# Kernel tuning notes

Measured on AMD Instinct MI355X. Metric: run time of the kernel, lower is better.

The kernel has to match this reference:

```python
import jax, jax.numpy as jnp
import numpy as np

N = 8192
IN_F = 512
OUT_F = 256

def setup_inputs() -> dict:
    key = jax.random.key(0)
    k1, k2, k3 = jax.random.split(key, 3)
    A = jax.random.uniform(k1, (N, N), dtype=jnp.float32)
    X = jax.random.normal(k2, (N, IN_F), dtype=jnp.float32)
    init_range = np.sqrt(6.0 / (IN_F + OUT_F)).astype(np.float32)
    W = jax.random.uniform(k3, (IN_F, OUT_F), dtype=jnp.float32,
                           minval=-init_range, maxval=init_range)
    return {"weighted_adjacency_matrix": A, "feature_matrix": X, "weight": W}

def reference(weighted_adjacency_matrix, feature_matrix, weight):
    A = weighted_adjacency_matrix
    # d = (1 + row_sum(A))^{-1/2}; D^{-1/2} A D^{-1/2} via row/col broadcast scaling
    d = jax.lax.rsqrt(1.0 + jnp.sum(A, axis=1))            # [N]
    norm_adj = d[:, None] * A * d[None, :]                  # [N, N]
    support = feature_matrix @ weight                       # [N, out_features]
    return norm_adj @ support                               # [N, out_features]
```

## Files before the change

kernel.cpp:

```cpp
#include <hip/hip_runtime.h>
#include <hip/hip_bf16.h>
#include <stdint.h>

#define NROW 8192
#define INF  512
#define OUTF 256

typedef __attribute__((ext_vector_type(8))) short bf16x8;
typedef __attribute__((ext_vector_type(4))) float f32x4;

__device__ __forceinline__ unsigned short f2bf(float x) {
  union { float f; unsigned u; } v; v.f = x;
  unsigned r = v.u + 0x7fffu + ((v.u >> 16) & 1u);
  return (unsigned short)(r >> 16);
}
__device__ __forceinline__ unsigned short f2bf_fast(float x) {
  union { float f; unsigned u; } v; v.f = x;
  return (unsigned short)((v.u + 0x8000u) >> 16);
}
__device__ __forceinline__ float bf2f(unsigned short h) {
  union { unsigned u; float f; } v; v.u = ((unsigned)h) << 16;
  return v.f;
}

__device__ __forceinline__ void async_cp16(const void* g, void* l) {
  __builtin_amdgcn_global_load_lds((const __attribute__((address_space(1))) void*)g,
                                   (__attribute__((address_space(3))) void*)l,
                                   16, 0, 0);
}

__global__ __launch_bounds__(256) void k_rowsum(
    const float* __restrict__ A, float* __restrict__ dv) {
  int w = threadIdx.x >> 6, lane = threadIdx.x & 63;
  int row = blockIdx.x * 4 + w;
  const float4* ar = (const float4*)(A + (size_t)row * NROW);
  float s = 0.f;
  #pragma unroll 4
  for (int it = 0; it < NROW / 256; ++it) {
    float4 v = ar[it * 64 + lane];
    s += (v.x + v.y) + (v.z + v.w);
  }
  #pragma unroll
  for (int off = 32; off > 0; off >>= 1) s += __shfl_down(s, off, 64);
  if (lane == 0) dv[row] = rsqrtf(1.f + s);
}

__global__ __launch_bounds__(256) void k_convert_w(
    const float* __restrict__ W, unsigned short* __restrict__ WsT) {
  int idx = blockIdx.x * 256 + threadIdx.x;
  int k = idx >> 8, f = idx & 255;
  WsT[(size_t)f * INF + k] = f2bf(W[idx]);
}

__global__ __launch_bounds__(256, 2) void k_support_fx(
    const unsigned short* __restrict__ WsT,
    const float* __restrict__ X,
    const float* __restrict__ dv,
    unsigned short* __restrict__ YT) {
  __shared__ unsigned short lA[128 * 64];
  __shared__ unsigned short lB[128 * 64];
  const int t = threadIdx.x;
  const int w = t >> 6, lane = t & 63;
  const int m0 = blockIdx.x * 128;
  const int n0 = blockIdx.y * 128;
  const int rsub = lane >> 3, csub = lane & 7, swz = csub ^ rsub;
  const int lr = lane & 15, lq = lane >> 4, x7 = lane & 7;
  const int mw = (w >> 1) * 64, nw = (w & 1) * 64;

  const int xrow = t >> 1, xhalf = t & 1;
  const float4* xsrc = (const float4*)(X + (size_t)(n0 + xrow) * INF + xhalf * 32);

  f32x4 acc[4][4];
  #pragma unroll
  for (int i = 0; i < 4; ++i)
    #pragma unroll
    for (int j = 0; j < 4; ++j) acc[i][j] = f32x4{0.f, 0.f, 0.f, 0.f};

  const unsigned short* ga0 = WsT + (size_t)(m0 + w * 8 + rsub) * INF + swz * 8;

  for (int it = 0; it < INF / 64; ++it) {
    __syncthreads();
    #pragma unroll
    for (int i = 0; i < 4; ++i)
      async_cp16(ga0 + (size_t)(i * 32) * INF + it * 64, &lA[(i * 32 + w * 8) * 64]);
    #pragma unroll
    for (int u = 0; u < 8; ++u) {
      float4 v = xsrc[it * 16 + u];
      ushort4 b;
      b.x = f2bf(v.x); b.y = f2bf(v.y); b.z = f2bf(v.z); b.w = f2bf(v.w);
      int k = xhalf * 32 + u * 4;
      int chunk = k >> 3, klo = k & 7;
      int slot = chunk ^ (xrow & 7);
      *(ushort4*)&lB[xrow * 64 + (slot << 3) + klo] = b;
    }
    __syncthreads();
    #pragma unroll
    for (int ks = 0; ks < 2; ++ks) {
      bf16x8 af[4], bfv[4];
      #pragma unroll
      for (int mi = 0; mi < 4; ++mi)
        af[mi] = *(const bf16x8*)&lA[(mw + mi * 16 + lr) * 64 + (((ks * 4 + lq) ^ x7) << 3)];
      #pragma unroll
      for (int ni = 0; ni < 4; ++ni)
        bfv[ni] = *(const bf16x8*)&lB[(nw + ni * 16 + lr) * 64 + (((ks * 4 + lq) ^ x7) << 3)];
      #pragma unroll
      for (int mi = 0; mi < 4; ++mi)
        #pragma unroll
        for (int ni = 0; ni < 4; ++ni)
          acc[mi][ni] = __builtin_amdgcn_mfma_f32_16x16x32_bf16(
              af[mi], bfv[ni], acc[mi][ni], 0, 0, 0);
    }
  }
  #pragma unroll
  for (int mi = 0; mi < 4; ++mi) {
    #pragma unroll
    for (int ni = 0; ni < 4; ++ni) {
      f32x4 a = acc[mi][ni];
      int gr0 = m0 + mw + mi * 16 + lq * 4;
      int gc  = n0 + nw + ni * 16 + lr;
      float dd = dv[gc];
      #pragma unroll
      for (int r = 0; r < 4; ++r)
        YT[(size_t)(gr0 + r) * NROW + gc] = f2bf(dd * a[r]);
    }
  }
}

__global__ __launch_bounds__(256, 2) void k_gemm_main_f32a(
    const float* __restrict__ A,
    const unsigned short* __restrict__ YT,
    unsigned short* __restrict__ P) {
  __shared__ unsigned short lA[128 * 64];
  __shared__ unsigned short lB[256 * 64];
  const int t = threadIdx.x;
  const int w = t >> 6, lane = t & 63;
  const int m0 = blockIdx.x * 128;
  const int kz = blockIdx.y * 1024;
  const int rsub = lane >> 3, csub = lane & 7, swz = csub ^ rsub;
  const int lr = lane & 15, lq = lane >> 4, x7 = lane & 7;
  const int mw = (w & 1) * 64;
  const int nw = (w >> 1) * 128;

  const int arow = t >> 2, aq = t & 3;
  const int aklo = (aq & 1) * 4;

  f32x4 acc[4][8];
  #pragma unroll
  for (int i = 0; i < 4; ++i)
    #pragma unroll
    for (int j = 0; j < 8; ++j) acc[i][j] = f32x4{0.f, 0.f, 0.f, 0.f};

  const unsigned short* gb0 = YT + (size_t)(w * 8 + rsub) * NROW + kz + swz * 8;

  for (int it = 0; it < 16; ++it) {
    __syncthreads();
    #pragma unroll
    for (int i = 0; i < 8; ++i)
      async_cp16(gb0 + (size_t)(i * 32) * NROW + it * 64, &lB[(i * 32 + w * 8) * 64]);
    #pragma unroll
    for (int h = 0; h < 2; ++h) {
      int r = arow + h * 64;
      const float4* asrc = (const float4*)(A + (size_t)(m0 + r) * NROW + kz + it * 64);
      #pragma unroll
      for (int j = 0; j < 4; ++j) {
        float4 v = asrc[aq + 4 * j];
        ushort4 b;
        b.x = f2bf_fast(v.x); b.y = f2bf_fast(v.y);
        b.z = f2bf_fast(v.z); b.w = f2bf_fast(v.w);
        int chunk = (aq + 4 * j) >> 1;
        int slot = chunk ^ (r & 7);
        *(ushort4*)&lA[r * 64 + (slot << 3) + aklo] = b;
      }
    }
    __syncthreads();
    #pragma unroll
    for (int ks = 0; ks < 2; ++ks) {
      bf16x8 af[4], bfv[8];
      #pragma unroll
      for (int mi = 0; mi < 4; ++mi)
        af[mi] = *(const bf16x8*)&lA[(mw + mi * 16 + lr) * 64 + (((ks * 4 + lq) ^ x7) << 3)];
      #pragma unroll
      for (int ni = 0; ni < 8; ++ni)
        bfv[ni] = *(const bf16x8*)&lB[(nw + ni * 16 + lr) * 64 + (((ks * 4 + lq) ^ x7) << 3)];
      #pragma unroll
      for (int mi = 0; mi < 4; ++mi)
        #pragma unroll
        for (int ni = 0; ni < 8; ++ni)
          acc[mi][ni] = __builtin_amdgcn_mfma_f32_16x16x32_bf16(
              af[mi], bfv[ni], acc[mi][ni], 0, 0, 0);
    }
  }

  unsigned short* Pz = P + (size_t)blockIdx.y * NROW * OUTF;
  #pragma unroll
  for (int mi = 0; mi < 4; ++mi) {
    #pragma unroll
    for (int ni = 0; ni < 8; ++ni) {
      f32x4 a = acc[mi][ni];
      int gr0 = m0 + mw + mi * 16 + lq * 4;
      int gc  = nw + ni * 16 + lr;
      #pragma unroll
      for (int r = 0; r < 4; ++r)
        Pz[(size_t)(gr0 + r) * OUTF + gc] = f2bf_fast(a[r]);
    }
  }
}

__global__ __launch_bounds__(256) void k_reduce8(
    const ushort4* __restrict__ P4, const float* __restrict__ dv,
    float4* __restrict__ o4) {
  int q = blockIdx.x * 256 + threadIdx.x;
  const int QT = NROW * OUTF / 4;
  float4 s = {0.f, 0.f, 0.f, 0.f};
  #pragma unroll
  for (int z = 0; z < 8; ++z) {
    ushort4 v = P4[(size_t)z * QT + q];
    s.x += bf2f(v.x); s.y += bf2f(v.y); s.z += bf2f(v.z); s.w += bf2f(v.w);
  }
  float dd = dv[q >> 6];
  s.x *= dd; s.y *= dd; s.z *= dd; s.w *= dd;
  o4[q] = s;
}

__global__ __launch_bounds__(256) void k_support_naive(
    const float* __restrict__ X, const float* __restrict__ W,
    const float* __restrict__ dv, float* __restrict__ Y) {
  __shared__ float lX[INF];
  int i = blockIdx.x;
  for (int k = threadIdx.x; k < INF; k += 256) lX[k] = X[(size_t)i * INF + k];
  __syncthreads();
  int f = threadIdx.x;
  float s = 0.f;
  for (int k = 0; k < INF; ++k) s += lX[k] * W[(size_t)k * OUTF + f];
  Y[(size_t)i * OUTF + f] = dv[i] * s;
}

__global__ __launch_bounds__(256) void k_main_naive(
    const float* __restrict__ A, const float* __restrict__ Y,
    const float* __restrict__ dv, float* __restrict__ out) {
  __shared__ float lA[256];
  int i = blockIdx.x, f = threadIdx.x;
  float s = 0.f;
  for (int jb = 0; jb < NROW; jb += 256) {
    __syncthreads();
    lA[threadIdx.x] = A[(size_t)i * NROW + jb + threadIdx.x];
    __syncthreads();
    for (int jj = 0; jj < 256; ++jj) s += lA[jj] * Y[(size_t)(jb + jj) * OUTF + f];
  }
  out[(size_t)i * OUTF + f] = dv[i] * s;
}

extern "C" void kernel_launch(void* const* d_in, const int* in_sizes, int n_in,
                              void* d_out, int out_size, void* d_ws, size_t ws_size,
                              hipStream_t stream) {
  const float* A = (const float*)d_in[0];
  const float* X = (const float*)d_in[1];
  const float* W = (const float*)d_in[2];
  float* out = (float*)d_out;

  const size_t SZ_YT  = (size_t)OUTF * NROW * 2;
  const size_t SZ_WST = (size_t)OUTF * INF * 2;
  const size_t SZ_D   = (size_t)NROW * 4;
  const size_t SZ_P   = (size_t)8 * NROW * OUTF * 2;
  const size_t NEED = SZ_YT + SZ_WST + SZ_D + SZ_P;

  char* p = (char*)d_ws;
  if (ws_size >= NEED) {
    unsigned short* YT  = (unsigned short*)p; p += SZ_YT;
    unsigned short* WsT = (unsigned short*)p; p += SZ_WST;
    float* dv = (float*)p; p += SZ_D;
    unsigned short* P = (unsigned short*)p;

    k_convert_w<<<dim3(512), dim3(256), 0, stream>>>(W, WsT);
    k_rowsum<<<dim3(2048), dim3(256), 0, stream>>>(A, dv);
    k_support_fx<<<dim3(2, 64), dim3(256), 0, stream>>>(WsT, X, dv, YT);
    k_gemm_main_f32a<<<dim3(64, 8), dim3(256), 0, stream>>>(A, YT, P);
    k_reduce8<<<dim3(2048), dim3(256), 0, stream>>>((const ushort4*)P, dv, (float4*)out);
  } else {
    float* dv = (float*)p; p += SZ_D;
    float* Y  = (float*)p;
    k_rowsum<<<dim3(2048), dim3(256), 0, stream>>>(A, dv);
    k_support_naive<<<dim3(8192), dim3(256), 0, stream>>>(X, W, dv, Y);
    k_main_naive<<<dim3(8192), dim3(256), 0, stream>>>(A, Y, dv, out);
  }
}
```

Measured before the change: 455.8 us.

## Convert A to bf16 during rowsum and run main GEMM on bf16 A

The row-sum kernel now also writes a bf16 copy of the adjacency matrix into workspace. A new main GEMM then streams that bf16 copy directly into LDS with async copies, instead of loading fp32 A and converting it inside the GEMM. This is meant to make the main GEMM's A loads smaller and simpler and to drop the per-tile conversion work. In exchange it writes an extra 128 MB intermediate and needs a larger workspace, and the new GEMM loop has no overlap between loads and MFMA work.

After: 454.2 us. About the same (-0.4%).

```diff
diff --git a/kernel.cpp b/kernel.cpp
--- a/kernel.cpp
+++ b/kernel.cpp
@@ -27,6 +27,27 @@
   __builtin_amdgcn_global_load_lds((const __attribute__((address_space(1))) void*)g,
                                    (__attribute__((address_space(3))) void*)l,
                                    16, 0, 0);
+}
+
+__global__ __launch_bounds__(256) void k_rowsum_cvt(
+    const float* __restrict__ A, float* __restrict__ dv,
+    unsigned short* __restrict__ Abf) {
+  int w = threadIdx.x >> 6, lane = threadIdx.x & 63;
+  int row = blockIdx.x * 4 + w;
+  const float4* ar = (const float4*)(A + (size_t)row * NROW);
+  ushort4* br = (ushort4*)(Abf + (size_t)row * NROW);
+  float s = 0.f;
+  #pragma unroll 4
+  for (int it = 0; it < NROW / 256; ++it) {
+    float4 v = ar[it * 64 + lane];
+    s += (v.x + v.y) + (v.z + v.w);
+    ushort4 b;
+    b.x = f2bf(v.x); b.y = f2bf(v.y); b.z = f2bf(v.z); b.w = f2bf(v.w);
+    br[it * 64 + lane] = b;
+  }
+  #pragma unroll
+  for (int off = 32; off > 0; off >>= 1) s += __shfl_down(s, off, 64);
+  if (lane == 0) dv[row] = rsqrtf(1.f + s);
 }
 
 __global__ __launch_bounds__(256) void k_rowsum(
@@ -126,6 +147,72 @@
   }
 }
 
+__global__ __launch_bounds__(256, 2) void k_gemm_main_bf16a(
+    const unsigned short* __restrict__ Abf,
+    const unsigned short* __restrict__ YT,
+    unsigned short* __restrict__ P) {
+  __shared__ unsigned short lA[128 * 64];
+  __shared__ unsigned short lB[256 * 64];
+  const int t = threadIdx.x;
+  const int w = t >> 6, lane = t & 63;
+  const int m0 = blockIdx.x * 128;
+  const int kz = blockIdx.y * 1024;
+  const int rsub = lane >> 3, csub = lane & 7, swz = csub ^ rsub;
+  const int lr = lane & 15, lq = lane >> 4, x7 = lane & 7;
+  const int mw = (w & 1) * 64;
+  const int nw = (w >> 1) * 128;
+
+  f32x4 acc[4][8];
+  #pragma unroll
+  for (int i = 0; i < 4; ++i)
+    #pragma unroll
+    for (int j = 0; j < 8; ++j) acc[i][j] = f32x4{0.f, 0.f, 0.f, 0.f};
+
+  const unsigned short* ga0 = Abf + (size_t)(m0 + w * 8 + rsub) * NROW + kz + swz * 8;
+  const unsigned short* gb0 = YT + (size_t)(w * 8 + rsub) * NROW + kz + swz * 8;
+
+  for (int it = 0; it < 16; ++it) {
+    __syncthreads();
+    #pragma unroll
+    for (int i = 0; i < 8; ++i)
+      async_cp16(gb0 + (size_t)(i * 32) * NROW + it * 64, &lB[(i * 32 + w * 8) * 64]);
+    #pragma unroll
+    for (int i = 0; i < 4; ++i)
+      async_cp16(ga0 + (size_t)(i * 32) * NROW + it * 64, &lA[(i * 32 + w * 8) * 64]);
+    __syncthreads();
+    #pragma unroll
+    for (int ks = 0; ks < 2; ++ks) {
+      bf16x8 af[4], bfv[8];
+      #pragma unroll
+      for (int mi = 0; mi < 4; ++mi)
+        af[mi] = *(const bf16x8*)&lA[(mw + mi * 16 + lr) * 64 + (((ks * 4 + lq) ^ x7) << 3)];
+      #pragma unroll
+      for (int ni = 0; ni < 8; ++ni)
+        bfv[ni] = *(const bf16x8*)&lB[(nw + ni * 16 + lr) * 64 + (((ks * 4 + lq) ^ x7) << 3)];
+      #pragma unroll
+      for (int mi = 0; mi < 4; ++mi)
+        #pragma unroll
+        for (int ni = 0; ni < 8; ++ni)
+          acc[mi][ni] = __builtin_amdgcn_mfma_f32_16x16x32_bf16(
+              af[mi], bfv[ni], acc[mi][ni], 0, 0, 0);
+    }
+  }
+
+  unsigned short* Pz = P + (size_t)blockIdx.y * NROW * OUTF;
+  #pragma unroll
+  for (int mi = 0; mi < 4; ++mi) {
+    #pragma unroll
+    for (int ni = 0; ni < 8; ++ni) {
+      f32x4 a = acc[mi][ni];
+      int gr0 = m0 + mw + mi * 16 + lq * 4;
+      int gc  = nw + ni * 16 + lr;
+      #pragma unroll
+      for (int r = 0; r < 4; ++r)
+        Pz[(size_t)(gr0 + r) * OUTF + gc] = f2bf_fast(a[r]);
+    }
+  }
+}
+
 __global__ __launch_bounds__(256, 2) void k_gemm_main_f32a(
     const float* __restrict__ A,
     const unsigned short* __restrict__ YT,
@@ -262,10 +349,24 @@
   const size_t SZ_WST = (size_t)OUTF * INF * 2;
   const size_t SZ_D   = (size_t)NROW * 4;
   const size_t SZ_P   = (size_t)8 * NROW * OUTF * 2;
-  const size_t NEED = SZ_YT + SZ_WST + SZ_D + SZ_P;
+  const size_t SZ_ABF = (size_t)NROW * NROW * 2;
+  const size_t NEED_BASE = SZ_YT + SZ_WST + SZ_D + SZ_P;
+  const size_t NEED_FULL = NEED_BASE + SZ_ABF;
 
   char* p = (char*)d_ws;
-  if (ws_size >= NEED) {
+  if (ws_size >= NEED_FULL) {
+    unsigned short* YT  = (unsigned short*)p; p += SZ_YT;
+    unsigned short* WsT = (unsigned short*)p; p += SZ_WST;
+    float* dv = (float*)p; p += SZ_D;
+    unsigned short* P = (unsigned short*)p; p += SZ_P;
+    unsigned short* Abf = (unsigned short*)p;
+
+    k_convert_w<<<dim3(512), dim3(256), 0, stream>>>(W, WsT);
+    k_rowsum_cvt<<<dim3(2048), dim3(256), 0, stream>>>(A, dv, Abf);
+    k_support_fx<<<dim3(2, 64), dim3(256), 0, stream>>>(WsT, X, dv, YT);
+    k_gemm_main_bf16a<<<dim3(64, 8), dim3(256), 0, stream>>>(Abf, YT, P);
+    k_reduce8<<<dim3(2048), dim3(256), 0, stream>>>((const ushort4*)P, dv, (float4*)out);
+  } else if (ws_size >= NEED_BASE) {
     unsigned short* YT  = (unsigned short*)p; p += SZ_YT;
     unsigned short* WsT = (unsigned short*)p; p += SZ_WST;
     float* dv = (float*)p; p += SZ_D;
```
